# Optimization experiments

Measured on AMD Instinct MI355X. Metric: run time of the kernel, lower is better.

Reference implementation:

```python
import jax, jax.numpy as jnp
import numpy as np

N_NODES = 100000
N_EDGES = 1600000
K = 10
ALPHA = 0.1


def setup_inputs() -> dict:
    key = jax.random.key(0)
    k1, k2, k3, k4 = jax.random.split(key, 4)
    m, nhid, m_y = 256, 64, 64
    x = jax.random.normal(k1, (N_NODES, m), dtype=jnp.float32)
    W1 = jax.random.normal(k2, (nhid, m), dtype=jnp.float32) * (1.0 / np.sqrt(m))
    b1 = jnp.zeros((nhid,), dtype=jnp.float32)
    W2 = jax.random.normal(k3, (m_y, nhid), dtype=jnp.float32) * (1.0 / np.sqrt(nhid))
    b2 = jnp.zeros((m_y,), dtype=jnp.float32)
    edge_index = jax.random.randint(k4, (2, N_EDGES), 0, N_NODES, dtype=jnp.int64)
    return {"x": x, "W1": W1, "b1": b1, "W2": W2, "b2": b2, "edge_index": edge_index}


def reference(x, W1, b1, W2, b2, edge_index):
    N = x.shape[0]
    # MLP (dropout is identity at inference)
    h0 = jax.nn.relu(x @ W1.T + b1) @ W2.T + b2  # [N, m_y]

    # GCN normalization with self loops (PyG gcn_norm, symmetric)
    loops = jnp.arange(N, dtype=edge_index.dtype)
    src = jnp.concatenate([edge_index[0], loops])  # message sources (x_j)
    dst = jnp.concatenate([edge_index[1], loops])  # aggregation targets
    ones = jnp.ones(src.shape, dtype=h0.dtype)
    deg = jax.ops.segment_sum(ones, dst, num_segments=N)  # in-degree incl. self loop
    dinv = jnp.where(deg > 0, jax.lax.rsqrt(deg), 0.0)
    norm = dinv[src] * dinv[dst]  # [E+N]

    # APPNP: h <- (1-alpha) * A_hat h + alpha * h0, K iterations
    def step(h, _):
        msg = norm[:, None] * h[src]                      # gather + scale, [E+N, m_y]
        agg = jax.ops.segment_sum(msg, dst, num_segments=N)  # scatter-add
        return (1.0 - ALPHA) * agg + ALPHA * h0, None

    h, _ = jax.lax.scan(step, h0, None, length=K)
    return h
```

## Files before the change

kernel.cpp:

```cpp
#include <hip/hip_runtime.h>
#include <hip/hip_bf16.h>
#include <hip/hip_fp16.h>

#define N_NODES 100000
#define N_EDGES 1600000
#define KITER   10
#define ALPHA   0.1f
#define MX      256
#define MH      64
#define MY      64

#define N_SBLK ((N_NODES + 255) / 256)
#define NPART   8
#define PART_SZ ((N_NODES + NPART - 1) / NPART)
#define PULLROW_BLOCKS (N_NODES / 8)
#define CSTRIDE 64

typedef __attribute__((ext_vector_type(8))) short bf16x8;
typedef __attribute__((ext_vector_type(4))) float f32x4;
typedef unsigned int uint32;

static __device__ __forceinline__ float us2f(unsigned short u) {
    union { unsigned int i; float f; } v; v.i = ((unsigned int)u) << 16; return v.f;
}
static __device__ __forceinline__ unsigned short f2us(float f) {
    union { float f; unsigned int i; } v; v.f = f;
    unsigned int x = v.i;
    unsigned int r = (x + 0x7fffu + ((x >> 16) & 1u)) >> 16;
    return (unsigned short)r;
}
static __device__ __forceinline__ float loadf(const void* p, size_t i, int f32) {
    return f32 ? ((const float*)p)[i] : us2f(((const unsigned short*)p)[i]);
}
static __device__ __forceinline__ float2 u2f2(uint32 u) {
    __half2 h; *(uint32*)&h = u; return __half22float2(h);
}
static __device__ __forceinline__ uint32 f22u(float x, float y) {
    __half2 h = __floats2half2_rn(x, y); return *(uint32*)&h;
}

__global__ __launch_bounds__(256) void detect_kernel(
    const void* __restrict__ x, const int* __restrict__ ei, int* __restrict__ flags)
{
    __shared__ int cnt_weird, cnt_nz_odd;
    const int tid = threadIdx.x;
    if (tid == 0) { cnt_weird = 0; cnt_nz_odd = 0; }
    __syncthreads();
    const unsigned short* xu = (const unsigned short*)x;
    int w = 0, nz = 0;
    for (int i = tid; i < 512; i += 256) {
        unsigned e = (xu[2 * i] >> 7) & 0xFFu;
        if (e != 0u && (e < 105u || e > 141u)) w++;
        if (ei[2 * i + 1] != 0) nz++;
    }
    atomicAdd(&cnt_weird, w);
    atomicAdd(&cnt_nz_odd, nz);
    __syncthreads();
    if (tid == 0) {
        flags[0] = (cnt_weird > 64) ? 1 : 0;
        flags[1] = (cnt_nz_odd == 0) ? 1 : 0;
    }
}

__global__ __launch_bounds__(256) void convw_kernel(
    const void* __restrict__ W1, const void* __restrict__ W2,
    const int* __restrict__ flags,
    unsigned short* __restrict__ Wf1, unsigned short* __restrict__ Wf2)
{
    const int i = blockIdx.x * 256 + threadIdx.x;
    const int f32 = flags[0];
    if (i < MH * MX) {
        unsigned short v = f32 ? f2us(((const float*)W1)[i])
                               : ((const unsigned short*)W1)[i];
        const int row = i >> 8, k = i & 255;
        const int cb = row >> 4, l16 = row & 15;
        const int s = k >> 5, quad = (k >> 3) & 3, j = k & 7;
        Wf1[(((s * 4 + cb) * 64) + quad * 16 + l16) * 8 + j] = v;
    }
    if (i < MY * MH) {
        unsigned short v = f32 ? f2us(((const float*)W2)[i])
                               : ((const unsigned short*)W2)[i];
        const int row = i >> 6, k = i & 63;
        const int cb = row >> 4, l16 = row & 15;
        const int s = k >> 5, quad = (k >> 3) & 3, j = k & 7;
        Wf2[(((s * 4 + cb) * 64) + quad * 16 + l16) * 8 + j] = v;
    }
}

#define H1S_LD 72
__global__ __launch_bounds__(256, 1) void mlp3_kernel(
    const void* __restrict__ x,
    const unsigned short* __restrict__ Wf1,
    const void* __restrict__ b1,
    const unsigned short* __restrict__ Wf2,
    const void* __restrict__ b2,
    const int* __restrict__ flags,
    const float* __restrict__ dinv,
    float* __restrict__ h0,
    __half* __restrict__ h0h,
    __half* __restrict__ u0h)
{
    __shared__ unsigned short Hs[4][16][H1S_LD];

    const int f32  = flags[0];
    const int tid  = threadIdx.x;
    const int wave = tid >> 6;
    const int lane = tid & 63;
    const int l16  = lane & 15;
    const int quad = lane >> 4;

    const int gw   = blockIdx.x * 4 + wave;
    const int base = gw * 16;
    if (base >= N_NODES) return;
    const int arow = min(base + l16, N_NODES - 1);

    bf16x8 a[8];
    if (f32) {
        const float* xf = (const float*)x;
        #pragma unroll
        for (int h = 0; h < 2; ++h) {
            float4 xa[8];
            #pragma unroll
            for (int s = 0; s < 4; ++s) {
                const float* p = xf + (size_t)arow * MX + (h * 4 + s) * 32 + quad * 8;
                xa[2 * s]     = *(const float4*)p;
                xa[2 * s + 1] = *(const float4*)(p + 4);
            }
            #pragma unroll
            for (int s = 0; s < 4; ++s) {
                bf16x8 t;
                t[0] = (short)f2us(xa[2 * s].x);     t[1] = (short)f2us(xa[2 * s].y);
                t[2] = (short)f2us(xa[2 * s].z);     t[3] = (short)f2us(xa[2 * s].w);
                t[4] = (short)f2us(xa[2 * s + 1].x); t[5] = (short)f2us(xa[2 * s + 1].y);
                t[6] = (short)f2us(xa[2 * s + 1].z); t[7] = (short)f2us(xa[2 * s + 1].w);
                a[h * 4 + s] = t;
            }
        }
    } else {
        const unsigned short* xu = (const unsigned short*)x;
        #pragma unroll
        for (int s = 0; s < 8; ++s)
            a[s] = *(const bf16x8*)(xu + (size_t)arow * MX + s * 32 + quad * 8);
    }

    const bf16x8* Wv1 = (const bf16x8*)Wf1;
    bf16x8 wf[8][4];
    #pragma unroll
    for (int s = 0; s < 8; ++s)
        #pragma unroll
        for (int cb = 0; cb < 4; ++cb)
            wf[s][cb] = Wv1[(s * 4 + cb) * 64 + lane];

    f32x4 acc[4] = {{0,0,0,0},{0,0,0,0},{0,0,0,0},{0,0,0,0}};
    #pragma unroll
    for (int s = 0; s < 8; ++s) {
        #pragma unroll
        for (int cb = 0; cb < 4; ++cb)
            acc[cb] = __builtin_amdgcn_mfma_f32_16x16x32_bf16(a[s], wf[s][cb], acc[cb], 0, 0, 0);
    }
    #pragma unroll
    for (int cb = 0; cb < 4; ++cb) {
        #pragma unroll
        for (int reg = 0; reg < 4; ++reg) {
            const int row = quad * 4 + reg;
            const int col = cb * 16 + l16;
            float v = fmaxf(acc[cb][reg] + loadf(b1, col, f32), 0.0f);
            Hs[wave][row][col] = f2us(v);
        }
    }
    const bf16x8* Wv2 = (const bf16x8*)Wf2;
    bf16x8 wf2[2][4];
    #pragma unroll
    for (int s = 0; s < 2; ++s)
        #pragma unroll
        for (int cb = 0; cb < 4; ++cb)
            wf2[s][cb] = Wv2[(s * 4 + cb) * 64 + lane];

    f32x4 acc2[4] = {{0,0,0,0},{0,0,0,0},{0,0,0,0},{0,0,0,0}};
    #pragma unroll
    for (int s = 0; s < 2; ++s) {
        const int k0 = s * 32 + quad * 8;
        bf16x8 af = *(const bf16x8*)&Hs[wave][l16][k0];
        #pragma unroll
        for (int cb = 0; cb < 4; ++cb)
            acc2[cb] = __builtin_amdgcn_mfma_f32_16x16x32_bf16(af, wf2[s][cb], acc2[cb], 0, 0, 0);
    }

    #pragma unroll
    for (int cb = 0; cb < 4; ++cb) {
        #pragma unroll
        for (int reg = 0; reg < 4; ++reg) {
            const int row = quad * 4 + reg;
            const int col = cb * 16 + l16;
            float v = acc2[cb][reg] + loadf(b2, col, f32);
            Hs[wave][row][col] = __half_as_ushort(__float2half(v));
        }
    }
    asm volatile("" ::: "memory");

    if (h0h) {
        #pragma unroll 4
        for (int r = 0; r < 16; ++r) {
            const int gr = base + r;
            const float dvd = dinv[gr];
            unsigned short hb = Hs[wave][r][lane];
            float f = __half2float(__ushort_as_half(hb));
            h0h[(size_t)gr * MY + lane] = __ushort_as_half(hb);
            u0h[(size_t)gr * MY + lane] = __float2half(dvd * f);
        }
        return;
    }

    if (h0) {
        #pragma unroll 4
        for (int r = 0; r < 16; ++r) {
            const int gr = base + r;
            if (gr < N_NODES)
                h0[(size_t)gr * MY + lane] =
                    __half2float(__ushort_as_half(Hs[wave][r][lane]));
        }
    }
}

__global__ __launch_bounds__(256) void zero_int_kernel(int* __restrict__ p, int n) {
    int i = blockIdx.x * 256 + threadIdx.x;
    if (i < n) p[i] = 0;
}

__global__ __launch_bounds__(256) void pack_kernel(
    const int* __restrict__ ei, const int* __restrict__ flags,
    int2* __restrict__ pairs)
{
    int e = blockIdx.x * 256 + threadIdx.x;
    if (e >= N_EDGES) return;
    int s, d;
    if (flags[1]) { s = ei[2 * e]; d = ei[2 * (N_EDGES + e)]; }
    else          { s = ei[e];     d = ei[N_EDGES + e]; }
    pairs[e] = make_int2(s, d);
}

__global__ __launch_bounds__(256) void degpack_kernel(
    const int* __restrict__ ei, const int* __restrict__ flags,
    int* __restrict__ deg)
{
    int e = blockIdx.x * 256 + threadIdx.x;
    if (e >= N_EDGES) return;
    int d = flags[1] ? ei[2 * (N_EDGES + e)] : ei[N_EDGES + e];
    atomicAdd(&deg[d], 1);
}

__global__ __launch_bounds__(256) void dinv_kernel(
    const int* __restrict__ deg, float* __restrict__ dinv)
{
    int i = blockIdx.x * 256 + threadIdx.x;
    if (i < N_NODES) dinv[i] = rsqrtf((float)(deg[i] + 1));
}

__global__ __launch_bounds__(256) void scan_partial_kernel(
    const int* __restrict__ deg, int* __restrict__ bsum)
{
    __shared__ int red[256];
    const int b = blockIdx.x;
    const int i = b * 256 + threadIdx.x;
    red[threadIdx.x] = (i < N_NODES) ? deg[i] : 0;
    __syncthreads();
    for (int s = 128; s > 0; s >>= 1) {
        if (threadIdx.x < s) red[threadIdx.x] += red[threadIdx.x + s];
        __syncthreads();
    }
    if (threadIdx.x == 0) bsum[b] = red[0];
}

__global__ __launch_bounds__(256) void scan_block_kernel(
    const int* __restrict__ bsum, int* __restrict__ boff)
{
    __shared__ int vals[N_SBLK];
    for (int i = threadIdx.x; i < N_SBLK; i += 256) vals[i] = bsum[i];
    __syncthreads();
    if (threadIdx.x == 0) {
        int run = 0;
        for (int i = 0; i < N_SBLK; ++i) { int v = vals[i]; vals[i] = run; run += v; }
    }
    __syncthreads();
    for (int i = threadIdx.x; i < N_SBLK; i += 256) boff[i] = vals[i];
}

__global__ __launch_bounds__(256) void rowptr_kernel(
    const int* __restrict__ deg, const int* __restrict__ boff,
    int* __restrict__ rowptr, int* __restrict__ fill)
{
    __shared__ int sc[256];
    const int b = blockIdx.x;
    const int i = b * 256 + threadIdx.x;
    const int v = (i < N_NODES) ? deg[i] : 0;
    sc[threadIdx.x] = v;
    __syncthreads();
    #pragma unroll
    for (int s = 1; s < 256; s <<= 1) {
        int t = (threadIdx.x >= s) ? sc[threadIdx.x - s] : 0;
        __syncthreads();
        sc[threadIdx.x] += t;
        __syncthreads();
    }
    const int incl = sc[threadIdx.x];
    if (i < N_NODES) { rowptr[i] = boff[b] + incl - v; fill[i] = 0; }
    if (i == N_NODES - 1) rowptr[N_NODES] = boff[b] + incl;
}

__global__ __launch_bounds__(256) void fillfix_kernel(
    const int2* __restrict__ pairs, int* __restrict__ fill,
    int* __restrict__ csr)
{
    const int part = blockIdx.x & (NPART - 1);
    const int g    = blockIdx.x >> 3;
    const int G    = gridDim.x >> 3;
    const int lo   = part * PART_SZ;
    for (int e = g * 256 + threadIdx.x; e < N_EDGES; e += G * 256) {
        int2 p = pairs[e];
        if ((unsigned)(p.y - lo) < (unsigned)PART_SZ) {
            int pos = atomicAdd(&fill[p.y], 1);
            if (pos < CSTRIDE) csr[(size_t)p.y * CSTRIDE + pos] = p.x;
        }
    }
}

__global__ __launch_bounds__(256) void fill_kernel(
    const int* __restrict__ ei, const int* __restrict__ flags,
    const float* __restrict__ dinv, const int* __restrict__ rowptr,
    int* __restrict__ fill, int2* __restrict__ csr)
{
    int e = blockIdx.x * 256 + threadIdx.x;
    if (e >= N_EDGES) return;
    int s, d;
    if (flags[1]) { s = ei[2 * e]; d = ei[2 * (N_EDGES + e)]; }
    else          { s = ei[e];     d = ei[N_EDGES + e]; }
    float w = (1.0f - ALPHA) * dinv[s] * dinv[d];
    int pos = rowptr[d] + atomicAdd(&fill[d], 1);
    csr[pos] = make_int2(s, __float_as_int(w));
}

#define RACC(c) do {                                                   \
    float2 v_ = u2f2(u[(size_t)(c) * 32 + col]);                       \
    ax += v_.x; ay += v_.y; } while (0)

__global__ __launch_bounds__(256) void pullrow_kernel(
    const int* __restrict__ fill, const int* __restrict__ csr,
    const float* __restrict__ dinv,
    const __half* __restrict__ h0h, const __half* __restrict__ uin,
    __half* __restrict__ uout,
    const int* __restrict__ flags, void* __restrict__ outp, int write_out)
{
    const int tid  = threadIdx.x;
    const int wave = tid >> 6;
    const int lane = tid & 63;
    const int slot = lane >> 5;
    const int col  = lane & 31;
    const int n    = blockIdx.x * 8 + wave * 2 + slot;

    const uint32* u = (const uint32*)uin;

    const float dvd = dinv[n];
    const size_t qi = (size_t)n * 32 + col;
    const uint32 usw = u[qi];
    const uint32 h0w = ((const uint32*)h0h)[qi];

    int p = n * CSTRIDE;
    const int end = p + min(fill[n], CSTRIDE);
    float ax = 0.0f, ay = 0.0f;

    const int nb = (end - p) >> 3;
    if (nb > 0) {
        int c0 = csr[p + 0], c1 = csr[p + 1], c2 = csr[p + 2], c3 = csr[p + 3];
        int c4 = csr[p + 4], c5 = csr[p + 5], c6 = csr[p + 6], c7 = csr[p + 7];
        for (int b = 1; b < nb; ++b) {
            const int pb = p + 8 * b;
            int t0 = csr[pb + 0], t1 = csr[pb + 1], t2 = csr[pb + 2], t3 = csr[pb + 3];
            int t4 = csr[pb + 4], t5 = csr[pb + 5], t6 = csr[pb + 6], t7 = csr[pb + 7];
            RACC(c0); RACC(c1); RACC(c2); RACC(c3);
            RACC(c4); RACC(c5); RACC(c6); RACC(c7);
            c0 = t0; c1 = t1; c2 = t2; c3 = t3;
            c4 = t4; c5 = t5; c6 = t6; c7 = t7;
        }
        RACC(c0); RACC(c1); RACC(c2); RACC(c3);
        RACC(c4); RACC(c5); RACC(c6); RACC(c7);
        p += nb * 8;
    }
    for (; p < end; ++p) {
        int c = csr[p];
        RACC(c);
    }

    float2 us  = u2f2(usw);
    float2 h0v = u2f2(h0w);
    float rx = (1.0f - ALPHA) * dvd * (ax + us.x) + ALPHA * h0v.x;
    float ry = (1.0f - ALPHA) * dvd * (ay + us.y) + ALPHA * h0v.y;

    if (write_out) {
        if (flags[0]) {
            ((float2*)outp)[qi] = make_float2(rx, ry);
        } else {
            ((uint32*)outp)[qi] =
                (uint32)f2us(rx) | ((uint32)f2us(ry) << 16);
        }
    } else {
        ((uint32*)uout)[qi] = f22u(dvd * rx, dvd * ry);
    }
}

__global__ __launch_bounds__(256) void pull_kernel(
    const int* __restrict__ rowptr, const int2* __restrict__ csr,
    const float* __restrict__ dinv,
    const float* __restrict__ h0, const float* __restrict__ hin,
    float* __restrict__ hout,
    const int* __restrict__ flags, void* __restrict__ outp, int write_out)
{
    const int lane = threadIdx.x & 63;
    const int node = blockIdx.x * 4 + (threadIdx.x >> 6);
    if (node >= N_NODES) return;
    int p   = rowptr[node];
    const int end = rowptr[node + 1];
    float acc = 0.0f;
    for (; p + 3 < end; p += 4) {
        int2 e0 = csr[p], e1 = csr[p + 1], e2 = csr[p + 2], e3 = csr[p + 3];
        float v0 = hin[(size_t)e0.x * MY + lane];
        float v1 = hin[(size_t)e1.x * MY + lane];
        float v2 = hin[(size_t)e2.x * MY + lane];
        float v3 = hin[(size_t)e3.x * MY + lane];
        acc += __int_as_float(e0.y) * v0;
        acc += __int_as_float(e1.y) * v1;
        acc += __int_as_float(e2.y) * v2;
        acc += __int_as_float(e3.y) * v3;
    }
    for (; p < end; ++p) {
        int2 e = csr[p];
        acc += __int_as_float(e.y) * hin[(size_t)e.x * MY + lane];
    }
    const size_t o = (size_t)node * MY + lane;
    float dv = dinv[node];
    float r = acc + (1.0f - ALPHA) * dv * dv * hin[o] + ALPHA * h0[o];
    if (write_out) {
        if (flags[0]) ((float*)outp)[o] = r;
        else          ((unsigned short*)outp)[o] = f2us(r);
    } else {
        hout[o] = r;
    }
}

__global__ __launch_bounds__(256) void self_kernel(
    const float4* __restrict__ h0, const float4* __restrict__ hin,
    const float* __restrict__ dinv, float4* __restrict__ hout)
{
    int idx = blockIdx.x * 256 + threadIdx.x;
    if (idx >= N_NODES * (MY / 4)) return;
    int node = idx / (MY / 4);
    float d = dinv[node];
    float w = (1.0f - ALPHA) * d * d;
    float4 a = h0[idx], b = hin[idx];
    float4 o;
    o.x = ALPHA * a.x + w * b.x;
    o.y = ALPHA * a.y + w * b.y;
    o.z = ALPHA * a.z + w * b.z;
    o.w = ALPHA * a.w + w * b.w;
    hout[idx] = o;
}

__global__ __launch_bounds__(256) void edge_kernel(
    const int* __restrict__ ei, const int* __restrict__ flags,
    const float* __restrict__ dinv,
    const float* __restrict__ hin, float* __restrict__ hout)
{
    int lane = threadIdx.x & 63;
    int e = blockIdx.x * 4 + (threadIdx.x >> 6);
    if (e >= N_EDGES) return;
    int s, d;
    if (flags[1]) { s = ei[2 * e]; d = ei[2 * (N_EDGES + e)]; }
    else          { s = ei[e];     d = ei[N_EDGES + e]; }
    float w = (1.0f - ALPHA) * dinv[s] * dinv[d];
    atomicAdd(&hout[(size_t)d * MY + lane], w * hin[(size_t)s * MY + lane]);
}

__global__ __launch_bounds__(256) void out_kernel(
    const float* __restrict__ h, void* __restrict__ out, const int* __restrict__ flags)
{
    int idx = blockIdx.x * 256 + threadIdx.x;
    if (idx < N_NODES * MY) {
        float v = h[idx];
        if (flags[0]) ((float*)out)[idx] = v;
        else          ((unsigned short*)out)[idx] = f2us(v);
    }
}

#define ALIGN256(v) ((((size_t)(v)) + 255) & ~(size_t)255)

extern "C" void kernel_launch(void* const* d_in, const int* in_sizes, int n_in,
                              void* d_out, int out_size, void* d_ws, size_t ws_size,
                              hipStream_t stream)
{
    const void* x  = d_in[0];
    const void* W1 = d_in[1];
    const void* b1 = d_in[2];
    const void* W2 = d_in[3];
    const void* b2 = d_in[4];
    const int*  ei = (const int*)d_in[5];

    const size_t HN = (size_t)N_NODES * MY;

    char* base = (char*)d_ws;
    int*    flags  = (int*)base;                    base += 256;
    float*  dinv   = (float*)base;                  base += ALIGN256((size_t)N_NODES * 4);
    int*    deg    = (int*)base;                    base += ALIGN256((size_t)N_NODES * 4);
    int*    rowptr = (int*)base;                    base += ALIGN256(((size_t)N_NODES + 4) * 4);
    int*    fill   = (int*)base;                    base += ALIGN256((size_t)N_NODES * 4);
    int*    bsum   = (int*)base;                    base += ALIGN256(((size_t)N_SBLK + 4) * 4);
    int*    boff   = (int*)base;                    base += ALIGN256(((size_t)N_SBLK + 4) * 4);
    unsigned short* Wf1 = (unsigned short*)base;    base += ALIGN256((size_t)MH * MX * 2);
    unsigned short* Wf2 = (unsigned short*)base;    base += ALIGN256((size_t)MY * MH * 2);
    char* big = base;

    char* t2 = big;
    int*    csrF  = (int*)t2;       t2 += ALIGN256((size_t)N_NODES * CSTRIDE * 4);
    __half* h0h   = (__half*)t2;    t2 += ALIGN256(HN * 2);
    __half* uA    = (__half*)t2;    t2 += ALIGN256(HN * 2);
    __half* uB    = (__half*)t2;    t2 += ALIGN256(HN * 2);
    int2*   pairs = (int2*)t2;      t2 += ALIGN256((size_t)N_EDGES * 8);
    const size_t need_t2 = (size_t)(t2 - (char*)d_ws);

    char* t1 = big;
    int2*   csr1 = (int2*)t1;       t1 += ALIGN256((size_t)N_EDGES * 8);
    float*  h0   = (float*)t1;      t1 += ALIGN256(HN * 4);
    float*  hA32 = (float*)t1;      t1 += ALIGN256(HN * 4);
    float*  hB32 = (float*)t1;      t1 += ALIGN256(HN * 4);
    const size_t need_t1 = (size_t)(t1 - (char*)d_ws);

    const int tier = (ws_size >= need_t2) ? 2 : (ws_size >= need_t1 ? 1 : 0);

    detect_kernel<<<1, 256, 0, stream>>>(x, ei, flags);
    convw_kernel<<<(MH * MX + 255) / 256, 256, 0, stream>>>(W1, W2, flags, Wf1, Wf2);

    if (tier == 2) {
        zero_int_kernel<<<(N_NODES + 255) / 256, 256, 0, stream>>>(fill, N_NODES);
        pack_kernel<<<(N_EDGES + 255) / 256, 256, 0, stream>>>(ei, flags, pairs);
        fillfix_kernel<<<NPART * 256, 256, 0, stream>>>(pairs, fill, csrF);
        dinv_kernel<<<(N_NODES + 255) / 256, 256, 0, stream>>>(fill, dinv);
        mlp3_kernel<<<((N_NODES + 15) / 16 + 3) / 4, 256, 0, stream>>>(
            x, Wf1, b1, Wf2, b2, flags, dinv, (float*)nullptr, h0h, uA);

        const __half* uin = uA;
        __half* uout = uB;
        for (int k = 0; k < KITER; ++k) {
            int last = (k == KITER - 1) ? 1 : 0;
            pullrow_kernel<<<PULLROW_BLOCKS, 256, 0, stream>>>(
                fill, csrF, dinv, h0h, uin, uout, flags, d_out, last);
            uin = uout;
            uout = (uout == uA) ? uB : uA;
        }
    } else if (tier == 1) {
        zero_int_kernel<<<(N_NODES + 255) / 256, 256, 0, stream>>>(deg, N_NODES);
        degpack_kernel<<<(N_EDGES + 255) / 256, 256, 0, stream>>>(ei, flags, deg);
        dinv_kernel<<<(N_NODES + 255) / 256, 256, 0, stream>>>(deg, dinv);
        mlp3_kernel<<<((N_NODES + 15) / 16 + 3) / 4, 256, 0, stream>>>(
            x, Wf1, b1, Wf2, b2, flags, dinv, h0, (__half*)nullptr, (__half*)nullptr);
        scan_partial_kernel<<<N_SBLK, 256, 0, stream>>>(deg, bsum);
        scan_block_kernel<<<1, 256, 0, stream>>>(bsum, boff);
        rowptr_kernel<<<N_SBLK, 256, 0, stream>>>(deg, boff, rowptr, fill);
        fill_kernel<<<(N_EDGES + 255) / 256, 256, 0, stream>>>(
            ei, flags, dinv, rowptr, fill, csr1);

        const float* hin = h0;
        float* hout = hA32;
        for (int k = 0; k < KITER; ++k) {
            int last = (k == KITER - 1) ? 1 : 0;
            pull_kernel<<<(N_NODES + 3) / 4, 256, 0, stream>>>(
                rowptr, csr1, dinv, h0, hin, hout, flags, d_out, last);
            hin = hout;
            hout = (hout == hA32) ? hB32 : hA32;
        }
    } else {
        zero_int_kernel<<<(N_NODES + 255) / 256, 256, 0, stream>>>(deg, N_NODES);
        degpack_kernel<<<(N_EDGES + 255) / 256, 256, 0, stream>>>(ei, flags, deg);
        dinv_kernel<<<(N_NODES + 255) / 256, 256, 0, stream>>>(deg, dinv);
        mlp3_kernel<<<((N_NODES + 15) / 16 + 3) / 4, 256, 0, stream>>>(
            x, Wf1, b1, Wf2, b2, flags, dinv, h0, (__half*)nullptr, (__half*)nullptr);
        const float* hin = h0;
        float* hout = hA32;
        const int n_f4 = N_NODES * (MY / 4);
        for (int k = 0; k < KITER; ++k) {
            self_kernel<<<(n_f4 + 255) / 256, 256, 0, stream>>>(
                (const float4*)h0, (const float4*)hin, dinv, (float4*)hout);
            edge_kernel<<<(N_EDGES + 3) / 4, 256, 0, stream>>>(ei, flags, dinv, hin, hout);
            hin = hout;
            hout = (hout == hA32) ? hB32 : hA32;
        }
        out_kernel<<<(N_NODES * MY + 255) / 256, 256, 0, stream>>>(hin, d_out, flags);
    }
}
```

Measured before the change: 704.3 us.

## Bucket edges by destination partition and split each node's neighbors across half-waves

```diff
diff --git a/kernel.cpp b/kernel.cpp
--- a/kernel.cpp
+++ b/kernel.cpp
@@ -13,8 +13,8 @@
 #define N_SBLK ((N_NODES + 255) / 256)
 #define NPART   8
 #define PART_SZ ((N_NODES + NPART - 1) / NPART)
-#define PULLROW_BLOCKS (N_NODES / 8)
 #define CSTRIDE 64
+#define BCAP    220000
 
 typedef __attribute__((ext_vector_type(8))) short bf16x8;
 typedef __attribute__((ext_vector_type(4))) float f32x4;
@@ -227,16 +227,47 @@
     if (i < n) p[i] = 0;
 }
 
-__global__ __launch_bounds__(256) void pack_kernel(
+__global__ __launch_bounds__(256) void pack2_kernel(
     const int* __restrict__ ei, const int* __restrict__ flags,
-    int2* __restrict__ pairs)
-{
-    int e = blockIdx.x * 256 + threadIdx.x;
-    if (e >= N_EDGES) return;
-    int s, d;
-    if (flags[1]) { s = ei[2 * e]; d = ei[2 * (N_EDGES + e)]; }
-    else          { s = ei[e];     d = ei[N_EDGES + e]; }
-    pairs[e] = make_int2(s, d);
+    int2* __restrict__ bpairs, int* __restrict__ gcur)
+{
+    __shared__ int cnt[NPART];
+    __shared__ int basez[NPART];
+    const int tid = threadIdx.x;
+    const int e   = blockIdx.x * 256 + tid;
+    if (tid < NPART) cnt[tid] = 0;
+    __syncthreads();
+    int s = 0, d = 0, q = 0, r = 0;
+    const bool valid = (e < N_EDGES);
+    if (valid) {
+        if (flags[1]) { s = ei[2 * e]; d = ei[2 * (N_EDGES + e)]; }
+        else          { s = ei[e];     d = ei[N_EDGES + e]; }
+        q = d / PART_SZ;
+        r = atomicAdd(&cnt[q], 1);
+    }
+    __syncthreads();
+    if (tid < NPART) basez[tid] = atomicAdd(&gcur[tid], cnt[tid]);
+    __syncthreads();
+    if (valid) {
+        int pos = basez[q] + r;
+        if (pos < BCAP) bpairs[(size_t)q * BCAP + pos] = make_int2(s, d);
+    }
+}
+
+__global__ __launch_bounds__(256) void fillfix2_kernel(
+    const int2* __restrict__ bpairs, const int* __restrict__ gcur,
+    int* __restrict__ fill, int* __restrict__ csr)
+{
+    const int part = blockIdx.x & (NPART - 1);
+    const int g    = blockIdx.x >> 3;
+    const int G    = gridDim.x >> 3;
+    const int cnt  = min(gcur[part], BCAP);
+    const int2* bp = bpairs + (size_t)part * BCAP;
+    for (int e = g * 256 + threadIdx.x; e < cnt; e += G * 256) {
+        int2 p = bp[e];
+        int pos = atomicAdd(&fill[p.y], 1);
+        if (pos < CSTRIDE) csr[(size_t)p.y * CSTRIDE + pos] = p.x;
+    }
 }
 
 __global__ __launch_bounds__(256) void degpack_kernel(
@@ -305,23 +336,6 @@
     const int incl = sc[threadIdx.x];
     if (i < N_NODES) { rowptr[i] = boff[b] + incl - v; fill[i] = 0; }
     if (i == N_NODES - 1) rowptr[N_NODES] = boff[b] + incl;
-}
-
-__global__ __launch_bounds__(256) void fillfix_kernel(
-    const int2* __restrict__ pairs, int* __restrict__ fill,
-    int* __restrict__ csr)
-{
-    const int part = blockIdx.x & (NPART - 1);
-    const int g    = blockIdx.x >> 3;
-    const int G    = gridDim.x >> 3;
-    const int lo   = part * PART_SZ;
-    for (int e = g * 256 + threadIdx.x; e < N_EDGES; e += G * 256) {
-        int2 p = pairs[e];
-        if ((unsigned)(p.y - lo) < (unsigned)PART_SZ) {
-            int pos = atomicAdd(&fill[p.y], 1);
-            if (pos < CSTRIDE) csr[(size_t)p.y * CSTRIDE + pos] = p.x;
-        }
-    }
 }
 
 __global__ __launch_bounds__(256) void fill_kernel(
@@ -339,11 +353,7 @@
     csr[pos] = make_int2(s, __float_as_int(w));
 }
 
-#define RACC(c) do {                                                   \
-    float2 v_ = u2f2(u[(size_t)(c) * 32 + col]);                       \
-    ax += v_.x; ay += v_.y; } while (0)
-
-__global__ __launch_bounds__(256) void pullrow_kernel(
+__global__ __launch_bounds__(256) void pullrow2_kernel(
     const int* __restrict__ fill, const int* __restrict__ csr,
     const float* __restrict__ dinv,
     const __half* __restrict__ h0h, const __half* __restrict__ uin,
@@ -353,9 +363,9 @@
     const int tid  = threadIdx.x;
     const int wave = tid >> 6;
     const int lane = tid & 63;
-    const int slot = lane >> 5;
+    const int eh   = lane >> 5;
     const int col  = lane & 31;
-    const int n    = blockIdx.x * 8 + wave * 2 + slot;
+    const int n    = blockIdx.x * 4 + wave;
 
     const uint32* u = (const uint32*)uin;
 
@@ -364,46 +374,42 @@
     const uint32 usw = u[qi];
     const uint32 h0w = ((const uint32*)h0h)[qi];
 
-    int p = n * CSTRIDE;
-    const int end = p + min(fill[n], CSTRIDE);
+    const int deg = min(fill[n], CSTRIDE);
+    const int b   = n * CSTRIDE;
     float ax = 0.0f, ay = 0.0f;
 
-    const int nb = (end - p) >> 3;
-    if (nb > 0) {
-        int c0 = csr[p + 0], c1 = csr[p + 1], c2 = csr[p + 2], c3 = csr[p + 3];
-        int c4 = csr[p + 4], c5 = csr[p + 5], c6 = csr[p + 6], c7 = csr[p + 7];
-        for (int b = 1; b < nb; ++b) {
-            const int pb = p + 8 * b;
-            int t0 = csr[pb + 0], t1 = csr[pb + 1], t2 = csr[pb + 2], t3 = csr[pb + 3];
-            int t4 = csr[pb + 4], t5 = csr[pb + 5], t6 = csr[pb + 6], t7 = csr[pb + 7];
-            RACC(c0); RACC(c1); RACC(c2); RACC(c3);
-            RACC(c4); RACC(c5); RACC(c6); RACC(c7);
-            c0 = t0; c1 = t1; c2 = t2; c3 = t3;
-            c4 = t4; c5 = t5; c6 = t6; c7 = t7;
-        }
-        RACC(c0); RACC(c1); RACC(c2); RACC(c3);
-        RACC(c4); RACC(c5); RACC(c6); RACC(c7);
-        p += nb * 8;
-    }
-    for (; p < end; ++p) {
-        int c = csr[p];
-        RACC(c);
-    }
-
-    float2 us  = u2f2(usw);
-    float2 h0v = u2f2(h0w);
-    float rx = (1.0f - ALPHA) * dvd * (ax + us.x) + ALPHA * h0v.x;
-    float ry = (1.0f - ALPHA) * dvd * (ay + us.y) + ALPHA * h0v.y;
-
-    if (write_out) {
-        if (flags[0]) {
-            ((float2*)outp)[qi] = make_float2(rx, ry);
+    for (int i0 = 0; i0 < deg; i0 += 32) {
+        int c[16];
+        #pragma unroll
+        for (int j = 0; j < 16; ++j) {
+            const int idx = i0 + 2 * j + eh;
+            c[j] = csr[b + min(idx, deg - 1)];
+        }
+        #pragma unroll
+        for (int j = 0; j < 16; ++j) {
+            const int idx = i0 + 2 * j + eh;
+            float2 v = u2f2(u[(size_t)c[j] * 32 + col]);
+            if (idx < deg) { ax += v.x; ay += v.y; }
+        }
+    }
+    ax += __shfl_xor(ax, 32);
+    ay += __shfl_xor(ay, 32);
+
+    if (eh == 0) {
+        float2 us  = u2f2(usw);
+        float2 h0v = u2f2(h0w);
+        float rx = (1.0f - ALPHA) * dvd * (ax + us.x) + ALPHA * h0v.x;
+        float ry = (1.0f - ALPHA) * dvd * (ay + us.y) + ALPHA * h0v.y;
+        if (write_out) {
+            if (flags[0]) {
+                ((float2*)outp)[qi] = make_float2(rx, ry);
+            } else {
+                ((uint32*)outp)[qi] =
+                    (uint32)f2us(rx) | ((uint32)f2us(ry) << 16);
+            }
         } else {
-            ((uint32*)outp)[qi] =
-                (uint32)f2us(rx) | ((uint32)f2us(ry) << 16);
-        }
-    } else {
-        ((uint32*)uout)[qi] = f22u(dvd * rx, dvd * ry);
+            ((uint32*)uout)[qi] = f22u(dvd * rx, dvd * ry);
+        }
     }
 }
 
@@ -511,6 +517,7 @@
     int*    deg    = (int*)base;                    base += ALIGN256((size_t)N_NODES * 4);
     int*    rowptr = (int*)base;                    base += ALIGN256(((size_t)N_NODES + 4) * 4);
     int*    fill   = (int*)base;                    base += ALIGN256((size_t)N_NODES * 4);
+    int*    gcur   = (int*)base;                    base += 256;
     int*    bsum   = (int*)base;                    base += ALIGN256(((size_t)N_SBLK + 4) * 4);
     int*    boff   = (int*)base;                    base += ALIGN256(((size_t)N_SBLK + 4) * 4);
     unsigned short* Wf1 = (unsigned short*)base;    base += ALIGN256((size_t)MH * MX * 2);
@@ -518,11 +525,11 @@
     char* big = base;
 
     char* t2 = big;
-    int*    csrF  = (int*)t2;       t2 += ALIGN256((size_t)N_NODES * CSTRIDE * 4);
-    __half* h0h   = (__half*)t2;    t2 += ALIGN256(HN * 2);
-    __half* uA    = (__half*)t2;    t2 += ALIGN256(HN * 2);
-    __half* uB    = (__half*)t2;    t2 += ALIGN256(HN * 2);
-    int2*   pairs = (int2*)t2;      t2 += ALIGN256((size_t)N_EDGES * 8);
+    int*    csrF   = (int*)t2;      t2 += ALIGN256((size_t)N_NODES * CSTRIDE * 4);
+    __half* h0h    = (__half*)t2;   t2 += ALIGN256(HN * 2);
+    __half* uA     = (__half*)t2;   t2 += ALIGN256(HN * 2);
+    __half* uB     = (__half*)t2;   t2 += ALIGN256(HN * 2);
+    int2*   bpairs = (int2*)t2;     t2 += ALIGN256((size_t)NPART * BCAP * 8);
     const size_t need_t2 = (size_t)(t2 - (char*)d_ws);
 
     char* t1 = big;
@@ -539,8 +546,9 @@
 
     if (tier == 2) {
         zero_int_kernel<<<(N_NODES + 255) / 256, 256, 0, stream>>>(fill, N_NODES);
-        pack_kernel<<<(N_EDGES + 255) / 256, 256, 0, stream>>>(ei, flags, pairs);
-        fillfix_kernel<<<NPART * 256, 256, 0, stream>>>(pairs, fill, csrF);
+        zero_int_kernel<<<1, 256, 0, stream>>>(gcur, NPART);
+        pack2_kernel<<<(N_EDGES + 255) / 256, 256, 0, stream>>>(ei, flags, bpairs, gcur);
+        fillfix2_kernel<<<NPART * 256, 256, 0, stream>>>(bpairs, gcur, fill, csrF);
         dinv_kernel<<<(N_NODES + 255) / 256, 256, 0, stream>>>(fill, dinv);
         mlp3_kernel<<<((N_NODES + 15) / 16 + 3) / 4, 256, 0, stream>>>(
             x, Wf1, b1, Wf2, b2, flags, dinv, (float*)nullptr, h0h, uA);
@@ -549,7 +557,7 @@
         __half* uout = uB;
         for (int k = 0; k < KITER; ++k) {
             int last = (k == KITER - 1) ? 1 : 0;
-            pullrow_kernel<<<PULLROW_BLOCKS, 256, 0, stream>>>(
+            pullrow2_kernel<<<N_NODES / 4, 256, 0, stream>>>(
                 fill, csrF, dinv, h0h, uin, uout, flags, d_out, last);
             uin = uout;
             uout = (uout == uA) ? uB : uA;
```

Result: slower. 849.0 us (+20.5%).
